# Performance work log

Measured on AMD Instinct MI355X. Metric: run time of the kernel, lower is better.

## Reference

```python
import jax, jax.numpy as jnp
import numpy as np

D_MODEL = 1024
N_SEQ = 2048
H = 16


def _rope_tables(d, n_seq):
    # theta_i = 10000^(-2i/d), i in [0, d/2)
    i = jnp.arange(d // 2, dtype=jnp.float32)
    theta = jnp.power(10000.0, -2.0 * i / d)                 # [d/2]
    ang = jnp.arange(n_seq, dtype=jnp.float32)[:, None] * theta[None, :]  # [S, d/2]
    cos = jnp.repeat(jnp.cos(ang), 2, axis=-1)               # [S, d] (cos duplicated per pair)
    s = jnp.sin(ang)
    sin = jnp.stack([s, -s], axis=-1).reshape(n_seq, d)      # [S, d] (+sin, -sin interleaved)
    return cos, sin


def _apply_rope(x, cos, sin):
    d = x.shape[-1]
    # swap adjacent pairs: (x0,x1,x2,x3,...) -> (x1,x0,x3,x2,...)
    x2 = x.reshape(x.shape[:-1] + (d // 2, 2))[..., ::-1].reshape(x.shape)
    return x * cos + x2 * sin


def setup_inputs() -> dict:
    key = jax.random.key(0)
    ks = jax.random.split(key, 8)
    B, S, D = 2, N_SEQ, D_MODEL
    scale = 1.0 / np.sqrt(D)
    return {
        "q": jax.random.normal(ks[0], (B, S, D), dtype=jnp.float32),
        "k": jax.random.normal(ks[1], (B, S, D), dtype=jnp.float32),
        "v": jax.random.normal(ks[2], (B, S, D), dtype=jnp.float32),
        "W_q": jax.random.normal(ks[3], (D, D), dtype=jnp.float32) * scale,
        "W_k": jax.random.normal(ks[4], (D, D), dtype=jnp.float32) * scale,
        "W_v": jax.random.normal(ks[5], (D, D), dtype=jnp.float32) * scale,
        "W_o": jax.random.normal(ks[6], (D, D), dtype=jnp.float32) * scale,
        "b_o": jax.random.normal(ks[7], (D,), dtype=jnp.float32) * scale,
    }


def reference(q, k, v, W_q, W_k, W_v, W_o, b_o):
    B, S, D = q.shape
    d_k = D // H
    cos, sin = _rope_tables(D, N_SEQ)

    query = _apply_rope(q @ W_q.T, cos, sin)  # RoPE over full d_model, pre head-split
    key_ = _apply_rope(k @ W_k.T, cos, sin)
    value = v @ W_v.T

    def split_heads(x):
        return x.reshape(B, S, H, d_k).transpose(0, 2, 1, 3)  # [B,H,S,dk]

    qh, kh, vh = split_heads(query), split_heads(key_), split_heads(value)

    scores = jnp.einsum("bhsd,bhtd->bhst", qh, kh) / jnp.sqrt(jnp.float32(d_k))
    attn = jax.nn.softmax(scores, axis=-1)
    y = jnp.einsum("bhst,bhtd->bhsd", attn, vh)               # [B,H,S,dk]
    y = y.transpose(0, 2, 1, 3).reshape(B, S, D)
    return y @ W_o.T + b_o
```

## Files before the change

kernel.cpp:

```cpp
#include <hip/hip_runtime.h>
#include <hip/hip_bf16.h>

using bf16 = __hip_bfloat16;
using bf16x8 = __attribute__((ext_vector_type(8))) short;
using f32x4 = __attribute__((ext_vector_type(4))) float;

#define LOG2E 1.44269504088896f

__device__ __forceinline__ void gload_lds16(const void* g, void* lds) {
    __builtin_amdgcn_global_load_lds(
        (const __attribute__((address_space(1))) void*)g,
        (__attribute__((address_space(3))) void*)lds, 16, 0, 0);
}

__device__ __forceinline__ float rsum16(float v) {
    v += __shfl_xor(v, 1);
    v += __shfl_xor(v, 2);
    v += __shfl_xor(v, 4);
    v += __shfl_xor(v, 8);
    return v;
}

struct __align__(16) BH8 { bf16 h[8]; };
struct __align__(8)  BH4 { bf16 h[4]; };

struct CvtArgs { const float* src[7]; BH8* dst[7]; };

__global__ __launch_bounds__(256) void cvt_all(CvtArgs ca) {
    int i = blockIdx.x * 256 + threadIdx.x;
    const float* src; BH8* dst; int off;
    if (i < 3 * 524288) {
        int w = i >> 19; off = i & 524287;
        src = ca.src[w]; dst = ca.dst[w];
    } else {
        int j = i - 3 * 524288;
        int w = 3 + (j >> 17); off = j & 131071;
        src = ca.src[w]; dst = ca.dst[w];
    }
    const float4* p = (const float4*)src + (size_t)off * 2;
    float4 a = p[0], b = p[1];
    BH8 r;
    r.h[0] = __float2bfloat16(a.x); r.h[1] = __float2bfloat16(a.y);
    r.h[2] = __float2bfloat16(a.z); r.h[3] = __float2bfloat16(a.w);
    r.h[4] = __float2bfloat16(b.x); r.h[5] = __float2bfloat16(b.y);
    r.h[6] = __float2bfloat16(b.z); r.h[7] = __float2bfloat16(b.w);
    dst[off] = r;
}

__global__ __launch_bounds__(256) void rope_tables(float* __restrict__ ct,
                                                   float* __restrict__ st) {
    int idx = blockIdx.x * 256 + threadIdx.x;
    if (idx >= 2048 * 512) return;
    int s = idx >> 9, i = idx & 511;
    float theta = exp2f((float)i * -0.0259525632413075f);
    float ang = (float)s * theta;
    ct[idx] = cosf(ang);
    st[idx] = sinf(ang);
}

struct ProjArgs {
    const bf16* A[3];
    const bf16* W[3];
    void* out[3];
    int mode[3];
};

template <int MF>
__global__ __launch_bounds__(256, 2) void gemm_bt(ProjArgs pa,
        const float* __restrict__ ct, const float* __restrict__ st,
        const float* __restrict__ bias) {
    constexpr int Kd = 1024;
    constexpr int BM = MF * 32;
    __shared__ __align__(16) bf16 As[BM * 32];
    __shared__ __align__(16) bf16 Bs[128 * 32];
    const int z = blockIdx.z;
    const bf16* __restrict__ A = pa.A[z];
    const bf16* __restrict__ W = pa.W[z];
    const int mode = pa.mode[z];
    const int tid = threadIdx.x, wid = tid >> 6, lane = tid & 63;
    const int g = lane >> 4, l15 = lane & 15;
    const int wm = wid >> 1, wn = wid & 1;
    const int m0 = blockIdx.y * BM, n0 = blockIdx.x * 128;
    f32x4 acc[MF][4] = {};
    const int sbyte = wid * 1024 + lane * 16;

    for (int kb = 0; kb < Kd; kb += 32) {
        __syncthreads();
#pragma unroll
        for (int r = 0; r < MF / 2; ++r) {
            int byte = sbyte + r * 4096;
            int row = byte >> 6, cb = byte & 63;
            int csrc = cb ^ (((row >> 1) & 3) << 4);
            gload_lds16((const char*)(A + (size_t)(m0 + row) * Kd + kb) + csrc,
                        (char*)As + wid * 1024 + r * 4096);
        }
#pragma unroll
        for (int r = 0; r < 2; ++r) {
            int byte = sbyte + r * 4096;
            int row = byte >> 6, cb = byte & 63;
            int csrc = cb ^ (((row >> 1) & 3) << 4);
            gload_lds16((const char*)(W + (size_t)(n0 + row) * Kd + kb) + csrc,
                        (char*)Bs + wid * 1024 + r * 4096);
        }
        __syncthreads();
        bf16x8 af[MF], bw[4];
#pragma unroll
        for (int i = 0; i < MF; ++i) {
            int ra = wm * (MF * 16) + i * 16 + l15;
            af[i] = *(const bf16x8*)((const char*)As + ra * 64 +
                                     ((g * 16) ^ (((ra >> 1) & 3) << 4)));
        }
#pragma unroll
        for (int j = 0; j < 4; ++j) {
            int rb = wn * 64 + j * 16 + l15;
            bw[j] = *(const bf16x8*)((const char*)Bs + rb * 64 +
                                     ((g * 16) ^ (((rb >> 1) & 3) << 4)));
        }
#pragma unroll
        for (int i = 0; i < MF; ++i)
#pragma unroll
            for (int j = 0; j < 4; ++j)
                acc[i][j] = __builtin_amdgcn_mfma_f32_16x16x32_bf16(af[i], bw[j], acc[i][j], 0, 0, 0);
    }

    if (mode == 0) {
        float* out = (float*)pa.out[z];
#pragma unroll
        for (int i = 0; i < MF; ++i) {
            int row = m0 + wm * (MF * 16) + i * 16 + g * 4;
#pragma unroll
            for (int j = 0; j < 4; ++j) {
                int col = n0 + wn * 64 + j * 16 + l15;
                float bv = bias[col];
#pragma unroll
                for (int r = 0; r < 4; ++r)
                    out[(size_t)(row + r) * 1024 + col] = acc[i][j][r] + bv;
            }
        }
    } else if (mode == 3) {
        bf16* out = (bf16*)pa.out[z];
#pragma unroll
        for (int i = 0; i < MF; ++i) {
            int m = m0 + wm * (MF * 16) + i * 16 + g * 4;
            int b = m >> 11, s = m & 2047;
#pragma unroll
            for (int j = 0; j < 4; ++j) {
                int col = n0 + wn * 64 + j * 16 + l15;
                int h = col >> 6, dv = col & 63;
                BH4 pk;
#pragma unroll
                for (int r = 0; r < 4; ++r) pk.h[r] = __float2bfloat16(acc[i][j][r]);
                *(BH4*)(out + (((size_t)(b * 16 + h)) * 64 + dv) * 2048 + s) = pk;
            }
        }
    } else {
        bf16* out = (bf16*)pa.out[z];
        float scl = (mode == 1) ? (0.125f * LOG2E) : 1.0f;
#pragma unroll
        for (int i = 0; i < MF; ++i) {
            int mrow = m0 + wm * (MF * 16) + i * 16 + g * 4;
#pragma unroll
            for (int j = 0; j < 4; ++j) {
                int col = n0 + wn * 64 + j * 16 + l15;
                int ci = col >> 1;
                float sgn = (col & 1) ? -1.0f : 1.0f;
                int h = col >> 6, dv = col & 63;
#pragma unroll
                for (int r = 0; r < 4; ++r) {
                    int m = mrow + r;
                    int b = m >> 11, s = m & 2047;
                    float vv = acc[i][j][r];
                    float pv = __shfl_xor(vv, 1);
                    float c = ct[s * 512 + ci], sn = st[s * 512 + ci];
                    float o = (vv * c + sgn * sn * pv) * scl;
                    out[(((size_t)(b * 16 + h)) * 2048 + s) * 64 + dv] = __float2bfloat16(o);
                }
            }
        }
    }
}

__global__ __launch_bounds__(256, 2) void attn_fwd(
        const bf16* __restrict__ Qh, const bf16* __restrict__ Kh,
        const bf16* __restrict__ Vt, bf16* __restrict__ Y) {
    __shared__ __align__(16) bf16 Ks[2][64 * 64];
    __shared__ __align__(16) bf16 Vs[2][64 * 64];
    __shared__ __align__(16) bf16 Ps[4][32 * 64];
    const int tid = threadIdx.x, wid = tid >> 6, lane = tid & 63;
    const int g = lane >> 4, l15 = lane & 15;
    const int lin = blockIdx.y * 16 + blockIdx.x;
    const int swz = (lin & 7) * 64 + (lin >> 3);
    const int bh = swz >> 4, qt = swz & 15;
    const int q0 = qt * 128 + wid * 32;
    const bf16* Qb = Qh + (size_t)bh * 2048 * 64;
    const bf16* Kb = Kh + (size_t)bh * 2048 * 64;
    const bf16* Vb = Vt + (size_t)bh * 64 * 2048;

    bf16x8 aq[2][2];
#pragma unroll
    for (int ar = 0; ar < 2; ++ar)
#pragma unroll
        for (int kk = 0; kk < 2; ++kk)
            aq[ar][kk] = *(const bf16x8*)(Qb + (size_t)(q0 + ar * 16 + l15) * 64 + kk * 32 + g * 8);

    f32x4 yacc[2][4] = {};
    float lrow[2][4] = {};

    const int sbyte = wid * 1024 + lane * 16;
    const int srow0 = sbyte >> 7, scb = sbyte & 127;
    const int csrc0 = scb ^ ((srow0 & 7) << 4);
    const int srow1 = (sbyte + 4096) >> 7;
    const int csrc1 = scb ^ ((srow1 & 7) << 4);

#define STAGE(T, BUF)                                                          \
    do {                                                                       \
        gload_lds16((const char*)(Kb + (size_t)((T) * 64 + srow0) * 64) + csrc0, \
                    (char*)&Ks[BUF][0] + wid * 1024);                          \
        gload_lds16((const char*)(Vb + (size_t)srow0 * 2048 + (T) * 64) + csrc0, \
                    (char*)&Vs[BUF][0] + wid * 1024);                          \
        gload_lds16((const char*)(Kb + (size_t)((T) * 64 + srow1) * 64) + csrc1, \
                    (char*)&Ks[BUF][0] + wid * 1024 + 4096);                   \
        gload_lds16((const char*)(Vb + (size_t)srow1 * 2048 + (T) * 64) + csrc1, \
                    (char*)&Vs[BUF][0] + wid * 1024 + 4096);                   \
    } while (0)

    STAGE(0, 0);

    for (int t = 0; t < 32; ++t) {
        __syncthreads();
        if (t < 31) STAGE(t + 1, (t + 1) & 1);
        const char* Kst = (const char*)&Ks[t & 1][0];
        const char* Vst = (const char*)&Vs[t & 1][0];

        f32x4 sacc[2][4] = {};
#pragma unroll
        for (int kk = 0; kk < 2; ++kk) {
            bf16x8 bk[4];
#pragma unroll
            for (int fr = 0; fr < 4; ++fr) {
                int c = fr * 16 + l15;
                bk[fr] = *(const bf16x8*)(Kst + c * 128 +
                                          ((kk * 64 + g * 16) ^ ((c & 7) << 4)));
            }
#pragma unroll
            for (int ar = 0; ar < 2; ++ar)
#pragma unroll
                for (int fr = 0; fr < 4; ++fr)
                    sacc[ar][fr] = __builtin_amdgcn_mfma_f32_16x16x32_bf16(aq[ar][kk], bk[fr], sacc[ar][fr], 0, 0, 0);
        }

#pragma unroll
        for (int ar = 0; ar < 2; ++ar)
#pragma unroll
            for (int rg = 0; rg < 4; ++rg) {
                float p0 = exp2f(sacc[ar][0][rg]);
                float p1 = exp2f(sacc[ar][1][rg]);
                float p2 = exp2f(sacc[ar][2][rg]);
                float p3 = exp2f(sacc[ar][3][rg]);
                lrow[ar][rg] += (p0 + p1) + (p2 + p3);
                int qr = ar * 16 + g * 4 + rg;
                char* pb = (char*)(&Ps[wid][0]) + qr * 128;
                int sw = (qr & 7) << 4;
                *(bf16*)(pb + ((l15 * 2) ^ sw))      = __float2bfloat16(p0);
                *(bf16*)(pb + ((32 + l15 * 2) ^ sw)) = __float2bfloat16(p1);
                *(bf16*)(pb + ((64 + l15 * 2) ^ sw)) = __float2bfloat16(p2);
                *(bf16*)(pb + ((96 + l15 * 2) ^ sw)) = __float2bfloat16(p3);
            }
        asm volatile("" ::: "memory");

#pragma unroll
        for (int kk = 0; kk < 2; ++kk) {
            bf16x8 ap[2], bv[4];
#pragma unroll
            for (int ar = 0; ar < 2; ++ar) {
                int rowp = ar * 16 + l15;
                ap[ar] = *(const bf16x8*)((const char*)(&Ps[wid][0]) + rowp * 128 +
                                          ((kk * 64 + g * 16) ^ ((rowp & 7) << 4)));
            }
#pragma unroll
            for (int dn = 0; dn < 4; ++dn) {
                int dvr = dn * 16 + l15;
                bv[dn] = *(const bf16x8*)(Vst + dvr * 128 +
                                          ((kk * 64 + g * 16) ^ ((dvr & 7) << 4)));
            }
#pragma unroll
            for (int ar = 0; ar < 2; ++ar)
#pragma unroll
                for (int dn = 0; dn < 4; ++dn)
                    yacc[ar][dn] = __builtin_amdgcn_mfma_f32_16x16x32_bf16(ap[ar], bv[dn], yacc[ar][dn], 0, 0, 0);
        }
        asm volatile("" ::: "memory");
    }

    const int b = bh >> 4, h = bh & 15;
#pragma unroll
    for (int ar = 0; ar < 2; ++ar)
#pragma unroll
        for (int rg = 0; rg < 4; ++rg) {
            float inv = 1.0f / rsum16(lrow[ar][rg]);
            int s = q0 + ar * 16 + g * 4 + rg;
            bf16* yp = Y + ((size_t)(b * 2048 + s)) * 1024 + h * 64;
#pragma unroll
            for (int dn = 0; dn < 4; ++dn)
                yp[dn * 16 + l15] = __float2bfloat16(yacc[ar][dn][rg] * inv);
        }
#undef STAGE
}

extern "C" void kernel_launch(void* const* d_in, const int* in_sizes, int n_in,
                              void* d_out, int out_size, void* d_ws, size_t ws_size,
                              hipStream_t stream) {
    const float* q  = (const float*)d_in[0];
    const float* k  = (const float*)d_in[1];
    const float* v  = (const float*)d_in[2];
    const float* Wq = (const float*)d_in[3];
    const float* Wk = (const float*)d_in[4];
    const float* Wv = (const float*)d_in[5];
    const float* Wo = (const float*)d_in[6];
    const float* bo = (const float*)d_in[7];

    const size_t MB = 1048576ull;
    if (ws_size < 72 * MB) return;
    char* p = (char*)d_ws;
    bf16* qb  = (bf16*)(p + 0 * MB);
    bf16* kb  = (bf16*)(p + 8 * MB);
    bf16* vb  = (bf16*)(p + 16 * MB);
    bf16* Wqb = (bf16*)(p + 24 * MB);
    bf16* Wkb = (bf16*)(p + 26 * MB);
    bf16* Wvb = (bf16*)(p + 28 * MB);
    bf16* Wob = (bf16*)(p + 30 * MB);
    bf16* Qh  = (bf16*)(p + 32 * MB);
    bf16* Kh  = (bf16*)(p + 40 * MB);
    bf16* Vt  = (bf16*)(p + 48 * MB);
    bf16* Yb  = (bf16*)(p + 56 * MB);
    float* ct = (float*)(p + 64 * MB);
    float* st = (float*)(p + 68 * MB);

    CvtArgs ca;
    ca.src[0] = q;  ca.dst[0] = (BH8*)qb;
    ca.src[1] = k;  ca.dst[1] = (BH8*)kb;
    ca.src[2] = v;  ca.dst[2] = (BH8*)vb;
    ca.src[3] = Wq; ca.dst[3] = (BH8*)Wqb;
    ca.src[4] = Wk; ca.dst[4] = (BH8*)Wkb;
    ca.src[5] = Wv; ca.dst[5] = (BH8*)Wvb;
    ca.src[6] = Wo; ca.dst[6] = (BH8*)Wob;
    cvt_all<<<8192, 256, 0, stream>>>(ca);
    rope_tables<<<4096, 256, 0, stream>>>(ct, st);

    ProjArgs pa;
    pa.A[0] = qb;  pa.A[1] = kb;  pa.A[2] = vb;
    pa.W[0] = Wqb; pa.W[1] = Wkb; pa.W[2] = Wvb;
    pa.out[0] = Qh; pa.out[1] = Kh; pa.out[2] = Vt;
    pa.mode[0] = 1; pa.mode[1] = 2; pa.mode[2] = 3;
    gemm_bt<4><<<dim3(8, 32, 3), 256, 0, stream>>>(pa, ct, st, nullptr);

    attn_fwd<<<dim3(16, 32), 256, 0, stream>>>(Qh, Kh, Vt, Yb);

    ProjArgs pf;
    pf.A[0] = Yb; pf.A[1] = Yb; pf.A[2] = Yb;
    pf.W[0] = Wob; pf.W[1] = Wob; pf.W[2] = Wob;
    pf.out[0] = d_out; pf.out[1] = d_out; pf.out[2] = d_out;
    pf.mode[0] = 0; pf.mode[1] = 0; pf.mode[2] = 0;
    gemm_bt<2><<<dim3(8, 64, 1), 256, 0, stream>>>(pf, ct, st, bo);
}
```

Baseline: 159.6 us.

## Compute transposed scores in registers, drop LDS staging for K, V and P

The attention kernel now computes S^T = K·Q^T with the MFMA so that each lane's score outputs already sit in the register layout needed for the P·V MFMA A-operand. This removes the LDS round-trip for P. K and V fragments are loaded straight from global memory into registers, with the next K tile prefetched, so the shared buffers and __syncthreads are gone. The row-sum reduction moves to a cross-group shuffle at the end. The trade is higher VGPR pressure and uncoalesced, uncached-in-LDS global loads of V that each wave repeats on its own.

Measured after the change: 203.6 us. +27.6%, slower.

```diff
diff --git a/kernel.cpp b/kernel.cpp
--- a/kernel.cpp
+++ b/kernel.cpp
@@ -11,14 +11,6 @@
     __builtin_amdgcn_global_load_lds(
         (const __attribute__((address_space(1))) void*)g,
         (__attribute__((address_space(3))) void*)lds, 16, 0, 0);
-}
-
-__device__ __forceinline__ float rsum16(float v) {
-    v += __shfl_xor(v, 1);
-    v += __shfl_xor(v, 2);
-    v += __shfl_xor(v, 4);
-    v += __shfl_xor(v, 8);
-    return v;
 }
 
 struct __align__(16) BH8 { bf16 h[8]; };
@@ -183,9 +175,6 @@
 __global__ __launch_bounds__(256, 2) void attn_fwd(
         const bf16* __restrict__ Qh, const bf16* __restrict__ Kh,
         const bf16* __restrict__ Vt, bf16* __restrict__ Y) {
-    __shared__ __align__(16) bf16 Ks[2][64 * 64];
-    __shared__ __align__(16) bf16 Vs[2][64 * 64];
-    __shared__ __align__(16) bf16 Ps[4][32 * 64];
     const int tid = threadIdx.x, wid = tid >> 6, lane = tid & 63;
     const int g = lane >> 4, l15 = lane & 15;
     const int lin = blockIdx.y * 16 + blockIdx.x;
@@ -198,113 +187,107 @@
 
     bf16x8 aq[2][2];
 #pragma unroll
-    for (int ar = 0; ar < 2; ++ar)
+    for (int qfr = 0; qfr < 2; ++qfr)
 #pragma unroll
         for (int kk = 0; kk < 2; ++kk)
-            aq[ar][kk] = *(const bf16x8*)(Qb + (size_t)(q0 + ar * 16 + l15) * 64 + kk * 32 + g * 8);
+            aq[qfr][kk] = *(const bf16x8*)(Qb + (size_t)(q0 + qfr * 16 + l15) * 64 + kk * 32 + g * 8);
+
+    int prow[4];
+#pragma unroll
+    for (int kfr = 0; kfr < 4; ++kfr)
+        prow[kfr] = ((kfr >> 1) << 5) + ((l15 >> 2) << 3) + ((kfr & 1) << 2) + (l15 & 3);
 
     f32x4 yacc[2][4] = {};
-    float lrow[2][4] = {};
-
-    const int sbyte = wid * 1024 + lane * 16;
-    const int srow0 = sbyte >> 7, scb = sbyte & 127;
-    const int csrc0 = scb ^ ((srow0 & 7) << 4);
-    const int srow1 = (sbyte + 4096) >> 7;
-    const int csrc1 = scb ^ ((srow1 & 7) << 4);
-
-#define STAGE(T, BUF)                                                          \
-    do {                                                                       \
-        gload_lds16((const char*)(Kb + (size_t)((T) * 64 + srow0) * 64) + csrc0, \
-                    (char*)&Ks[BUF][0] + wid * 1024);                          \
-        gload_lds16((const char*)(Vb + (size_t)srow0 * 2048 + (T) * 64) + csrc0, \
-                    (char*)&Vs[BUF][0] + wid * 1024);                          \
-        gload_lds16((const char*)(Kb + (size_t)((T) * 64 + srow1) * 64) + csrc1, \
-                    (char*)&Ks[BUF][0] + wid * 1024 + 4096);                   \
-        gload_lds16((const char*)(Vb + (size_t)srow1 * 2048 + (T) * 64) + csrc1, \
-                    (char*)&Vs[BUF][0] + wid * 1024 + 4096);                   \
-    } while (0)
-
-    STAGE(0, 0);
+    float lrow[2] = {0.f, 0.f};
+
+    bf16x8 kf[4][2];
+#pragma unroll
+    for (int kfr = 0; kfr < 4; ++kfr)
+#pragma unroll
+        for (int kk = 0; kk < 2; ++kk)
+            kf[kfr][kk] = *(const bf16x8*)(Kb + (size_t)prow[kfr] * 64 + kk * 32 + g * 8);
 
     for (int t = 0; t < 32; ++t) {
-        __syncthreads();
-        if (t < 31) STAGE(t + 1, (t + 1) & 1);
-        const char* Kst = (const char*)&Ks[t & 1][0];
-        const char* Vst = (const char*)&Vs[t & 1][0];
-
-        f32x4 sacc[2][4] = {};
-#pragma unroll
-        for (int kk = 0; kk < 2; ++kk) {
-            bf16x8 bk[4];
-#pragma unroll
-            for (int fr = 0; fr < 4; ++fr) {
-                int c = fr * 16 + l15;
-                bk[fr] = *(const bf16x8*)(Kst + c * 128 +
-                                          ((kk * 64 + g * 16) ^ ((c & 7) << 4)));
+        bf16x8 vf[4][2];
+#pragma unroll
+        for (int dn = 0; dn < 4; ++dn)
+#pragma unroll
+            for (int a = 0; a < 2; ++a)
+                vf[dn][a] = *(const bf16x8*)(Vb + (size_t)(dn * 16 + l15) * 2048 + t * 64 + a * 32 + g * 8);
+
+        f32x4 sacc[4][2] = {};
+#pragma unroll
+        for (int kk = 0; kk < 2; ++kk)
+#pragma unroll
+            for (int kfr = 0; kfr < 4; ++kfr)
+#pragma unroll
+                for (int qfr = 0; qfr < 2; ++qfr)
+                    sacc[kfr][qfr] = __builtin_amdgcn_mfma_f32_16x16x32_bf16(
+                        kf[kfr][kk], aq[qfr][kk], sacc[kfr][qfr], 0, 0, 0);
+
+        bf16x8 kn[4][2];
+        if (t < 31) {
+#pragma unroll
+            for (int kfr = 0; kfr < 4; ++kfr)
+#pragma unroll
+                for (int kk = 0; kk < 2; ++kk)
+                    kn[kfr][kk] = *(const bf16x8*)(Kb + (size_t)((t + 1) * 64 + prow[kfr]) * 64 + kk * 32 + g * 8);
+        }
+
+        bf16x8 ap[2][2];
+#pragma unroll
+        for (int qfr = 0; qfr < 2; ++qfr)
+#pragma unroll
+            for (int a = 0; a < 2; ++a) {
+                bf16 h[8];
+#pragma unroll
+                for (int r = 0; r < 4; ++r) {
+                    float x = exp2f(sacc[2 * a][qfr][r]);
+                    lrow[qfr] += x;
+                    h[r] = __float2bfloat16(x);
+                }
+#pragma unroll
+                for (int r = 0; r < 4; ++r) {
+                    float x = exp2f(sacc[2 * a + 1][qfr][r]);
+                    lrow[qfr] += x;
+                    h[4 + r] = __float2bfloat16(x);
+                }
+                ap[qfr][a] = *(const bf16x8*)h;
             }
-#pragma unroll
-            for (int ar = 0; ar < 2; ++ar)
-#pragma unroll
-                for (int fr = 0; fr < 4; ++fr)
-                    sacc[ar][fr] = __builtin_amdgcn_mfma_f32_16x16x32_bf16(aq[ar][kk], bk[fr], sacc[ar][fr], 0, 0, 0);
-        }
-
-#pragma unroll
-        for (int ar = 0; ar < 2; ++ar)
-#pragma unroll
-            for (int rg = 0; rg < 4; ++rg) {
-                float p0 = exp2f(sacc[ar][0][rg]);
-                float p1 = exp2f(sacc[ar][1][rg]);
-                float p2 = exp2f(sacc[ar][2][rg]);
-                float p3 = exp2f(sacc[ar][3][rg]);
-                lrow[ar][rg] += (p0 + p1) + (p2 + p3);
-                int qr = ar * 16 + g * 4 + rg;
-                char* pb = (char*)(&Ps[wid][0]) + qr * 128;
-                int sw = (qr & 7) << 4;
-                *(bf16*)(pb + ((l15 * 2) ^ sw))      = __float2bfloat16(p0);
-                *(bf16*)(pb + ((32 + l15 * 2) ^ sw)) = __float2bfloat16(p1);
-                *(bf16*)(pb + ((64 + l15 * 2) ^ sw)) = __float2bfloat16(p2);
-                *(bf16*)(pb + ((96 + l15 * 2) ^ sw)) = __float2bfloat16(p3);
-            }
-        asm volatile("" ::: "memory");
-
-#pragma unroll
-        for (int kk = 0; kk < 2; ++kk) {
-            bf16x8 ap[2], bv[4];
-#pragma unroll
-            for (int ar = 0; ar < 2; ++ar) {
-                int rowp = ar * 16 + l15;
-                ap[ar] = *(const bf16x8*)((const char*)(&Ps[wid][0]) + rowp * 128 +
-                                          ((kk * 64 + g * 16) ^ ((rowp & 7) << 4)));
-            }
-#pragma unroll
-            for (int dn = 0; dn < 4; ++dn) {
-                int dvr = dn * 16 + l15;
-                bv[dn] = *(const bf16x8*)(Vst + dvr * 128 +
-                                          ((kk * 64 + g * 16) ^ ((dvr & 7) << 4)));
-            }
-#pragma unroll
-            for (int ar = 0; ar < 2; ++ar)
+
+#pragma unroll
+        for (int a = 0; a < 2; ++a)
+#pragma unroll
+            for (int qfr = 0; qfr < 2; ++qfr)
 #pragma unroll
                 for (int dn = 0; dn < 4; ++dn)
-                    yacc[ar][dn] = __builtin_amdgcn_mfma_f32_16x16x32_bf16(ap[ar], bv[dn], yacc[ar][dn], 0, 0, 0);
-        }
-        asm volatile("" ::: "memory");
+                    yacc[qfr][dn] = __builtin_amdgcn_mfma_f32_16x16x32_bf16(
+                        ap[qfr][a], vf[dn][a], yacc[qfr][dn], 0, 0, 0);
+
+#pragma unroll
+        for (int kfr = 0; kfr < 4; ++kfr)
+#pragma unroll
+            for (int kk = 0; kk < 2; ++kk)
+                kf[kfr][kk] = kn[kfr][kk];
     }
 
     const int b = bh >> 4, h = bh & 15;
 #pragma unroll
-    for (int ar = 0; ar < 2; ++ar)
-#pragma unroll
-        for (int rg = 0; rg < 4; ++rg) {
-            float inv = 1.0f / rsum16(lrow[ar][rg]);
-            int s = q0 + ar * 16 + g * 4 + rg;
+    for (int qfr = 0; qfr < 2; ++qfr) {
+        float ls = lrow[qfr];
+        ls += __shfl_xor(ls, 16);
+        ls += __shfl_xor(ls, 32);
+#pragma unroll
+        for (int r = 0; r < 4; ++r) {
+            float lv = __shfl(ls, g * 4 + r);
+            float inv = 1.0f / lv;
+            int s = q0 + qfr * 16 + g * 4 + r;
             bf16* yp = Y + ((size_t)(b * 2048 + s)) * 1024 + h * 64;
 #pragma unroll
             for (int dn = 0; dn < 4; ++dn)
-                yp[dn * 16 + l15] = __float2bfloat16(yacc[ar][dn][rg] * inv);
-        }
-#undef STAGE
+                yp[dn * 16 + l15] = __float2bfloat16(yacc[qfr][dn][r] * inv);
+        }
+    }
 }
 
 extern "C" void kernel_launch(void* const* d_in, const int* in_sizes, int n_in,
```
